# Optimization experiments

Measured on AMD Instinct MI355X. Metric: run time of the kernel, lower is better.

Reference implementation:

```python
import jax, jax.numpy as jnp
import numpy as np

NEG_SLOPE = 0.2
EPS = 1e-16  # PyG softmax denominator epsilon


def add_self_loops(edge_index, num_nodes):
    loop = jnp.arange(num_nodes, dtype=edge_index.dtype)
    src = jnp.concatenate([edge_index[0], loop])
    dst = jnp.concatenate([edge_index[1], loop])
    return src, dst


def gat_conv(x, src, dst, W, att_src, att_dst, bias, num_nodes):
    H, C = att_src.shape
    h = (x @ W).reshape(num_nodes, H, C)            # [N,H,C]
    a_s = jnp.einsum('nhc,hc->nh', h, att_src)      # [N,H]
    a_d = jnp.einsum('nhc,hc->nh', h, att_dst)
    e = jax.nn.leaky_relu(a_s[src] + a_d[dst], NEG_SLOPE)  # [E,H]
    m = jax.ops.segment_max(e, dst, num_segments=num_nodes)
    e = jnp.exp(e - m[dst])
    s = jax.ops.segment_sum(e, dst, num_segments=num_nodes)
    alpha = e / (s[dst] + EPS)                      # [E,H]
    out = jax.ops.segment_sum(h[src] * alpha[:, :, None], dst,
                              num_segments=num_nodes)  # [N,H,C]
    return out.reshape(num_nodes, H * C) + bias


def setup_inputs() -> dict:
    key = jax.random.key(0)
    ks = jax.random.split(key, 10)
    N, E, F, Ch = 50000, 800000, 128, 64
    sc = lambda f: 1.0 / np.sqrt(f)
    return {
        'x': jax.random.normal(ks[0], (N, F), jnp.float32),
        'edge_index': jax.random.randint(ks[1], (2, E), 0, N, jnp.int64),
        'W1': jax.random.normal(ks[2], (F, 4 * Ch), jnp.float32) * sc(F),
        'att_src1': jax.random.normal(ks[3], (4, Ch), jnp.float32) * sc(Ch),
        'att_dst1': jax.random.normal(ks[4], (4, Ch), jnp.float32) * sc(Ch),
        'b1': jnp.zeros((4 * Ch,), jnp.float32),
        'W2': jax.random.normal(ks[5], (4 * Ch, Ch), jnp.float32) * sc(4 * Ch),
        'att_src2': jax.random.normal(ks[6], (1, Ch), jnp.float32) * sc(Ch),
        'att_dst2': jax.random.normal(ks[7], (1, Ch), jnp.float32) * sc(Ch),
        'b2': jnp.zeros((Ch,), jnp.float32),
    }


def reference(x, edge_index, W1, att_src1, att_dst1, b1, W2, att_src2, att_dst2, b2):
    N = x.shape[0]
    src, dst = add_self_loops(edge_index, N)
    # dropout layers are inference no-ops
    h = gat_conv(x, src, dst, W1, att_src1, att_dst1, b1, N)
    h = jax.nn.elu(h)
    out = gat_conv(h, src, dst, W2, att_src2, att_dst2, b2, N)
    return out
```

## Files before the change

### kernel.cpp

```cpp
#include <hip/hip_runtime.h>
#include <hip/hip_bf16.h>
#include <stdint.h>


typedef __attribute__((ext_vector_type(8))) short bf16x8;
typedef __attribute__((ext_vector_type(8))) unsigned short u16x8;
typedef __attribute__((ext_vector_type(4))) float f32x4;

__device__ __forceinline__ float bf2f(__hip_bfloat16 v) { return __bfloat162float(v); }
__device__ __forceinline__ float bfbits2f(unsigned short s) {
  union { uint32_t u; float f; } v; v.u = ((uint32_t)s) << 16; return v.f;
}
__device__ __forceinline__ unsigned short f2bfbits(float f) {
  union { float f; uint32_t u; } v; v.f = f;
  uint32_t u = v.u;
  return (unsigned short)((u + 0x7fffu + ((u >> 16) & 1u)) >> 16);
}

template <bool BF>
__device__ __forceinline__ float loadF(const void* p, size_t i) {
  if (BF) return bf2f(((const __hip_bfloat16*)p)[i]);
  return ((const float*)p)[i];
}
template <bool BF>
__device__ __forceinline__ void storeF(void* p, size_t i, float v) {
  if (BF) ((__hip_bfloat16*)p)[i] = __float2bfloat16(v);
  else    ((float*)p)[i] = v;
}
template <bool I64>
__device__ __forceinline__ int loadI(const void* p, size_t i) {
  if (I64) return (int)((const long long*)p)[i];
  return ((const int*)p)[i];
}
__device__ __forceinline__ float lrelu(float v) { return fmaxf(v, 0.2f * v); }

__global__ void detect_kernel(const uint32_t* __restrict__ xbits,
                              const uint32_t* __restrict__ eibits,
                              int* __restrict__ flags) {
  const int l = threadIdx.x;
  uint32_t u = xbits[l];
  uint32_t e = (u >> 23) & 0xffu;
  bool plausible = (e < 160u && e > 90u) || (u & 0x7fffffffu) == 0u;
  unsigned long long m1 = __ballot(plausible);
  bool z = (eibits[2 * l + 1] == 0u);
  unsigned long long m2 = __ballot(z);
  if (l == 0) {
    flags[0] = (__popcll(m1) < 32) ? 1 : 0;
    flags[1] = (m2 == ~0ULL) ? 1 : 0;
  }
}

__global__ __launch_bounds__(256) void prep_all(
    const void* __restrict__ x, unsigned short* __restrict__ xb, size_t nx,
    const void* __restrict__ W1, unsigned short* __restrict__ w1t, int K1, int N1,
    const void* __restrict__ W2, unsigned short* __restrict__ w2t, int K2, int N2,
    int nb_cast, int nb_t1, const int* __restrict__ flags) {
  const int b = blockIdx.x;
  const bool f = flags[0] != 0;
  if (b < nb_cast) {
    size_t i = ((size_t)b * 256 + threadIdx.x) * 4;
    if (i >= nx) return;
    ushort4 o;
    if (f) {
      o = *(const ushort4*)((const unsigned short*)x + i);
    } else {
      float4 v = *(const float4*)((const float*)x + i);
      o.x = f2bfbits(v.x); o.y = f2bfbits(v.y);
      o.z = f2bfbits(v.z); o.w = f2bfbits(v.w);
    }
    *(ushort4*)(xb + i) = o;
  } else if (b < nb_cast + nb_t1) {
    int idx = (b - nb_cast) * 256 + threadIdx.x;
    if (idx >= K1 * N1) return;
    int k = idx / N1, n = idx - k * N1;
    float v = f ? loadF<true>(W1, idx) : loadF<false>(W1, idx);
    w1t[(size_t)n * K1 + k] = f2bfbits(v);
  } else {
    int idx = (b - nb_cast - nb_t1) * 256 + threadIdx.x;
    if (idx >= K2 * N2) return;
    int k = idx / N2, n = idx - k * N2;
    float v = f ? loadF<true>(W2, idx) : loadF<false>(W2, idx);
    w2t[(size_t)n * K2 + k] = f2bfbits(v);
  }
}

template <int KC, int NT, int HB>
__global__ __launch_bounds__(256, 4) void gemm_mfma_att(
    const unsigned short* __restrict__ A,
    const unsigned short* __restrict__ BT,
    unsigned short* __restrict__ C,
    const void* __restrict__ att_s, const void* __restrict__ att_d,
    float* __restrict__ as_o, float* __restrict__ ad_o,
    float* __restrict__ wself_o,
    int M, int Htot, const int* __restrict__ flags) {
  const int lane = threadIdx.x & 63;
  const int col = lane & 15;
  const int quad = lane >> 4;
  const int m0 = blockIdx.x * 64 + (threadIdx.x >> 6) * 16;
  const int n0 = blockIdx.y * (NT * 16);
  const int NCOL = Htot * 64;

  int gm = m0 + col;
  if (gm > M - 1) gm = M - 1;
  const unsigned short* arow = A + (size_t)gm * KC + quad * 8;
  const unsigned short* bbase = BT + (size_t)(n0 + col) * KC + quad * 8;

  f32x4 acc[NT] = {};
#pragma unroll
  for (int k0 = 0; k0 < KC; k0 += 32) {
    bf16x8 a = *(const bf16x8*)(arow + k0);
#pragma unroll
    for (int s = 0; s < NT; s++) {
      bf16x8 b = *(const bf16x8*)(bbase + (size_t)s * 16 * KC + k0);
      acc[s] = __builtin_amdgcn_mfma_f32_16x16x32_bf16(a, b, acc[s], 0, 0, 0);
    }
  }
#pragma unroll
  for (int s = 0; s < NT; s++)
#pragma unroll
    for (int r = 0; r < 4; r++) {
      int m = m0 + quad * 4 + r;
      if (m < M) C[(size_t)m * NCOL + n0 + s * 16 + col] = f2bfbits(acc[s][r]);
    }
  const int SC = NT / HB;
  const bool f = flags[0] != 0;
#pragma unroll
  for (int h = 0; h < HB; h++) {
    const int gh = blockIdx.y * HB + h;
    float ps[4] = {0.f, 0.f, 0.f, 0.f};
    float pd[4] = {0.f, 0.f, 0.f, 0.f};
#pragma unroll
    for (int j = 0; j < SC; j++) {
      int s = h * SC + j;
      int ci = gh * 64 + j * 16 + col;
      float av = f ? loadF<true>(att_s, ci) : loadF<false>(att_s, ci);
      float dv = f ? loadF<true>(att_d, ci) : loadF<false>(att_d, ci);
#pragma unroll
      for (int r = 0; r < 4; r++) {
        ps[r] += acc[s][r] * av;
        pd[r] += acc[s][r] * dv;
      }
    }
#pragma unroll
    for (int o = 1; o < 16; o <<= 1) {
#pragma unroll
      for (int r = 0; r < 4; r++) {
        ps[r] += __shfl_xor(ps[r], o);
        pd[r] += __shfl_xor(pd[r], o);
      }
    }
    if (col == 0) {
#pragma unroll
      for (int r = 0; r < 4; r++) {
        int m = m0 + quad * 4 + r;
        if (m < M) {
          as_o[m * Htot + gh] = ps[r];
          ad_o[m * Htot + gh] = pd[r];
          wself_o[m * Htot + gh] = __expf(lrelu(ps[r] + pd[r]));
        }
      }
    }
  }
}

__global__ void hist_kernel(const void* __restrict__ ei, int E,
                            int* __restrict__ deg, const int* __restrict__ flags) {
  int e = blockIdx.x * blockDim.x + threadIdx.x;
  if (e >= E) return;
  int d = flags[1] ? loadI<true>(ei, (size_t)E + e) : loadI<false>(ei, (size_t)E + e);
  atomicAdd(&deg[d], 1);
}

__global__ __launch_bounds__(256) void scan_block_sums(const int* __restrict__ deg,
                                                       int* __restrict__ bsum, int n) {
  __shared__ int buf[256];
  const int t = threadIdx.x;
  const int i = blockIdx.x * 256 + t;
  buf[t] = (i < n) ? deg[i] : 0;
  __syncthreads();
  for (int o = 128; o > 0; o >>= 1) {
    if (t < o) buf[t] += buf[t + o];
    __syncthreads();
  }
  if (t == 0) bsum[blockIdx.x] = buf[0];
}

__global__ __launch_bounds__(256) void scan_bsums(int* __restrict__ bsum, int nb) {
  __shared__ int buf[256];
  const int t = threadIdx.x;
  int orig = (t < nb) ? bsum[t] : 0;
  buf[t] = orig;
  __syncthreads();
  for (int o = 1; o < 256; o <<= 1) {
    int v = (t >= o) ? buf[t - o] : 0;
    __syncthreads();
    buf[t] += v;
    __syncthreads();
  }
  if (t < nb) bsum[t] = buf[t] - orig;
}

__global__ __launch_bounds__(256) void scan_finalize(const int* __restrict__ deg,
                                                     const int* __restrict__ bsum,
                                                     int* __restrict__ row_start, int n) {
  __shared__ int buf[256];
  const int t = threadIdx.x;
  const int i = blockIdx.x * 256 + t;
  int v = (i < n) ? deg[i] : 0;
  buf[t] = v;
  __syncthreads();
  for (int o = 1; o < 256; o <<= 1) {
    int x = (t >= o) ? buf[t - o] : 0;
    __syncthreads();
    buf[t] += x;
    __syncthreads();
  }
  if (i < n) row_start[i + 1] = bsum[blockIdx.x] + buf[t];
  if (i == 0) row_start[0] = 0;
}

__global__ void scatter_edges(const void* __restrict__ ei, int E,
                              const int* __restrict__ row_start,
                              int* __restrict__ cursor, int* __restrict__ col_src,
                              int* __restrict__ col_dst,
                              const int* __restrict__ flags) {
  int e = blockIdx.x * blockDim.x + threadIdx.x;
  if (e >= E) return;
  int s, d;
  if (flags[1]) { s = loadI<true>(ei, e);  d = loadI<true>(ei, (size_t)E + e); }
  else          { s = loadI<false>(ei, e); d = loadI<false>(ei, (size_t)E + e); }
  int pos = atomicAdd(&cursor[d], 1);
  int idx = row_start[d] + pos;
  col_src[idx] = s;
  col_dst[idx] = d;
}

__global__ __launch_bounds__(256) void weight4(
    const int* __restrict__ col_src, const int* __restrict__ col_dst,
    const float4* __restrict__ as4, const float4* __restrict__ ad4,
    float4* __restrict__ wbuf, int E) {
  int e = blockIdx.x * 256 + threadIdx.x;
  if (e >= E) return;
  float4 a = as4[col_src[e]];
  float4 b = ad4[col_dst[e]];
  float4 w;
  w.x = __expf(lrelu(a.x + b.x));
  w.y = __expf(lrelu(a.y + b.y));
  w.z = __expf(lrelu(a.z + b.z));
  w.w = __expf(lrelu(a.w + b.w));
  wbuf[e] = w;
}

__global__ __launch_bounds__(256) void weight1(
    const int* __restrict__ col_src, const int* __restrict__ col_dst,
    const float* __restrict__ as_, const float* __restrict__ ad_,
    float* __restrict__ wbuf, int E) {
  int e = blockIdx.x * 256 + threadIdx.x;
  if (e >= E) return;
  wbuf[e] = __expf(lrelu(as_[col_src[e]] + ad_[col_dst[e]]));
}

__global__ __launch_bounds__(256) void aggregate4(
    const unsigned short* __restrict__ h_in,
    const float* __restrict__ wselfA,
    const float* __restrict__ wbuf,
    const int* __restrict__ row_start, const int* __restrict__ col_src,
    const void* __restrict__ bias,
    unsigned short* __restrict__ out,
    int N, const int* __restrict__ flags) {
  const int dst = blockIdx.x * 4 + (threadIdx.x >> 6);
  if (dst >= N) return;
  const int l = threadIdx.x & 63;
  const int j = l & 31;
  const int half = l >> 5;
  const int h = j >> 3;
  const int rs = row_start[dst];
  const int dg = row_start[dst + 1] - rs;
  const float ws = wselfA[dst * 4 + h];

  float a[8];
  {
    u16x8 sv = *(const u16x8*)(h_in + (size_t)dst * 256 + 8 * j);
    const float s = half ? 0.f : ws;
#pragma unroll
    for (int r = 0; r < 8; r++) a[r] = s * bfbits2f(sv[r]);
  }
  float p = 0.f;
#pragma unroll 4
  for (int i = 0; i < dg; i += 2) {
    const int ii = i + half;
    const bool act = ii < dg;
    const int idx = rs + (act ? ii : (dg - 1));
    const int sn = col_src[idx];
    const float w = act ? wbuf[(size_t)idx * 4 + h] : 0.f;
    p += w;
    u16x8 sv = *(const u16x8*)(h_in + (size_t)sn * 256 + 8 * j);
#pragma unroll
    for (int r = 0; r < 8; r++) a[r] += w * bfbits2f(sv[r]);
  }
#pragma unroll
  for (int r = 0; r < 8; r++) a[r] += __shfl_xor(a[r], 32);
  p += __shfl_xor(p, 32);

  if (half == 0) {
    const float inv = 1.0f / (p + ws + 1e-16f);
    const bool f = flags[0] != 0;
    u16x8 ov;
#pragma unroll
    for (int r = 0; r < 8; r++) {
      float b = f ? loadF<true>(bias, 8 * j + r) : loadF<false>(bias, 8 * j + r);
      float o = a[r] * inv + b;
      o = o > 0.f ? o : __expf(o) - 1.f;
      ov[r] = f2bfbits(o);
    }
    *(u16x8*)(out + (size_t)dst * 256 + 8 * j) = ov;
  }
}

__global__ __launch_bounds__(256) void aggregate1(
    const unsigned short* __restrict__ h_in,
    const float* __restrict__ wselfA,
    const float* __restrict__ wbuf,
    const int* __restrict__ row_start, const int* __restrict__ col_src,
    const void* __restrict__ bias,
    void* __restrict__ out, int N, const int* __restrict__ flags) {
  const int dst = blockIdx.x * 4 + (threadIdx.x >> 6);
  if (dst >= N) return;
  const int l = threadIdx.x & 63;
  const int el = l & 7;
  const int slot = l >> 3;
  const int rs = row_start[dst];
  const int dg = row_start[dst + 1] - rs;
  const float ws = wselfA[dst];

  float a[8];
  {
    u16x8 sv = *(const u16x8*)(h_in + (size_t)dst * 64 + 8 * el);
    const float s = (slot == 0) ? ws : 0.f;
#pragma unroll
    for (int r = 0; r < 8; r++) a[r] = s * bfbits2f(sv[r]);
  }
  float p = 0.f;
#pragma unroll 2
  for (int i = slot; i < dg; i += 8) {
    const int sn = col_src[rs + i];
    const float w = wbuf[rs + i];
    p += w;
    u16x8 sv = *(const u16x8*)(h_in + (size_t)sn * 64 + 8 * el);
#pragma unroll
    for (int r = 0; r < 8; r++) a[r] += w * bfbits2f(sv[r]);
  }
#pragma unroll
  for (int o = 8; o < 64; o <<= 1) {
#pragma unroll
    for (int r = 0; r < 8; r++) a[r] += __shfl_xor(a[r], o);
    p += __shfl_xor(p, o);
  }

  if (slot == 0) {
    const float inv = 1.0f / (p + ws + 1e-16f);
    const bool f = flags[0] != 0;
    float o[8];
#pragma unroll
    for (int r = 0; r < 8; r++) {
      float b = f ? loadF<true>(bias, 8 * el + r) : loadF<false>(bias, 8 * el + r);
      o[r] = a[r] * inv + b;
    }
    const size_t ob = (size_t)dst * 64 + 8 * el;
    if (f) {
      u16x8 ov;
#pragma unroll
      for (int r = 0; r < 8; r++) ov[r] = f2bfbits(o[r]);
      *(u16x8*)((unsigned short*)out + ob) = ov;
    } else {
      float4 v0, v1;
      v0.x = o[0]; v0.y = o[1]; v0.z = o[2]; v0.w = o[3];
      v1.x = o[4]; v1.y = o[5]; v1.z = o[6]; v1.w = o[7];
      *(float4*)((float*)out + ob) = v0;
      *(float4*)((float*)out + ob + 4) = v1;
    }
  }
}

extern "C" void kernel_launch(void* const* d_in, const int* in_sizes, int n_in,
                              void* d_out, int out_size, void* d_ws, size_t ws_size,
                              hipStream_t stream) {
  const void* x    = d_in[0];
  const void* ei   = d_in[1];
  const void* W1   = d_in[2];
  const void* as1w = d_in[3];
  const void* ad1w = d_in[4];
  const void* b1   = d_in[5];
  const void* W2   = d_in[6];
  const void* as2w = d_in[7];
  const void* ad2w = d_in[8];
  const void* b2   = d_in[9];

  const int N  = out_size / 64;
  const int F  = in_sizes[0] / N;
  const int E  = in_sizes[1] / 2;
  const int H1 = in_sizes[3] / 64;
  const int D1 = H1 * 64;
  const int D2 = 64;

  size_t off = 0;
  auto alloc = [&](size_t bytes) -> void* {
    void* p = (char*)d_ws + off;
    off += (bytes + 255) & ~(size_t)255;
    return p;
  };
  int* flags = (int*)alloc(2 * sizeof(int));
  __hip_bfloat16* h1 = (__hip_bfloat16*)alloc((size_t)N * D1 * 2);
  __hip_bfloat16* x2 = (__hip_bfloat16*)alloc((size_t)N * D1 * 2);
  __hip_bfloat16* h2 = h1;
  unsigned short* xb  = (unsigned short*)alloc((size_t)N * F * 2);
  unsigned short* w1t = (unsigned short*)alloc((size_t)D1 * F * 2);
  unsigned short* w2t = (unsigned short*)alloc((size_t)D2 * D1 * 2);
  float* as1 = (float*)alloc((size_t)N * H1 * 4);
  float* ad1 = (float*)alloc((size_t)N * H1 * 4);
  float* wself1 = (float*)alloc((size_t)N * H1 * 4);
  float* as2 = (float*)alloc((size_t)N * 4);
  float* ad2 = (float*)alloc((size_t)N * 4);
  float* wself2 = (float*)alloc((size_t)N * 4);
  int* zero_region = (int*)alloc((size_t)2 * N * 4);
  int* deg = zero_region;
  int* cursor = zero_region + N;
  int* row_start = (int*)alloc((size_t)(N + 1) * 4);
  int* col_src = (int*)alloc((size_t)E * 4);
  int* col_dst = (int*)alloc((size_t)E * 4);
  float* wbuf = (float*)alloc((size_t)E * 4 * 4);
  int* bsum = (int*)alloc((size_t)256 * 4);
  (void)ws_size; (void)n_in;

  const int nb = (N + 255) / 256;
  const int eb = (E + 255) / 256;
  const int db = (N + 3) / 4;
  const int gb = (N + 63) / 64;

  detect_kernel<<<1, 64, 0, stream>>>((const uint32_t*)x, (const uint32_t*)ei, flags);
  hipMemsetAsync(zero_region, 0, (size_t)2 * N * 4, stream);
  hist_kernel<<<eb, 256, 0, stream>>>(ei, E, deg, flags);
  scan_block_sums<<<nb, 256, 0, stream>>>(deg, bsum, N);
  scan_bsums<<<1, 256, 0, stream>>>(bsum, nb);
  scan_finalize<<<nb, 256, 0, stream>>>(deg, bsum, row_start, N);
  scatter_edges<<<eb, 256, 0, stream>>>(ei, E, row_start, cursor, col_src, col_dst, flags);

  const size_t nx = (size_t)N * F;
  const int nb_cast = (int)((nx / 4 + 255) / 256);
  const int nb_t1 = (F * D1 + 255) / 256;
  const int nb_t2 = (D1 * D2 + 255) / 256;
  prep_all<<<nb_cast + nb_t1 + nb_t2, 256, 0, stream>>>(
      x, xb, nx, W1, w1t, F, D1, W2, w2t, D1, D2, nb_cast, nb_t1, flags);

  gemm_mfma_att<128, 8, 2><<<dim3(gb, 2), 256, 0, stream>>>(
      xb, w1t, (unsigned short*)h1, as1w, ad1w, as1, ad1, wself1, N, H1, flags);
  weight4<<<eb, 256, 0, stream>>>(col_src, col_dst, (const float4*)as1,
                                  (const float4*)ad1, (float4*)wbuf, E);
  aggregate4<<<db, 256, 0, stream>>>((const unsigned short*)h1, wself1, wbuf,
                                     row_start, col_src, b1,
                                     (unsigned short*)x2, N, flags);

  gemm_mfma_att<256, 4, 1><<<dim3(gb, 1), 256, 0, stream>>>(
      (const unsigned short*)x2, w2t, (unsigned short*)h2, as2w, ad2w,
      as2, ad2, wself2, N, 1, flags);
  weight1<<<eb, 256, 0, stream>>>(col_src, col_dst, as2, ad2, wbuf, E);
  aggregate1<<<db, 256, 0, stream>>>((const unsigned short*)h2, wself2, wbuf,
                                     row_start, col_src, b2, d_out, N, flags);
}
```

Baseline: 349.4 us.

## Slice aggregation across column blocks and store edge weights as per-head planes

Both aggregation kernels become one templated kernel. Each block now handles a 32-column slice of four destination nodes, so layer 1 launches 8x as many blocks and layer 2 launches 2x. Edge weights are written head-major, one plane per head, so each slice reads them contiguously, and each lane now handles four columns with 8 edge slots per wave instead of 2. The goal is more parallelism and smaller per-slice gathers, at the cost of re-reading col_src and the weights once per slice and using narrower 8-byte loads.

```diff
diff --git a/kernel.cpp b/kernel.cpp
--- a/kernel.cpp
+++ b/kernel.cpp
@@ -4,7 +4,6 @@
 
 
 typedef __attribute__((ext_vector_type(8))) short bf16x8;
-typedef __attribute__((ext_vector_type(8))) unsigned short u16x8;
 typedef __attribute__((ext_vector_type(4))) float f32x4;
 
 __device__ __forceinline__ float bf2f(__hip_bfloat16 v) { return __bfloat162float(v); }
@@ -21,11 +20,6 @@
 __device__ __forceinline__ float loadF(const void* p, size_t i) {
   if (BF) return bf2f(((const __hip_bfloat16*)p)[i]);
   return ((const float*)p)[i];
-}
-template <bool BF>
-__device__ __forceinline__ void storeF(void* p, size_t i, float v) {
-  if (BF) ((__hip_bfloat16*)p)[i] = __float2bfloat16(v);
-  else    ((float*)p)[i] = v;
 }
 template <bool I64>
 __device__ __forceinline__ int loadI(const void* p, size_t i) {
@@ -238,17 +232,15 @@
 __global__ __launch_bounds__(256) void weight4(
     const int* __restrict__ col_src, const int* __restrict__ col_dst,
     const float4* __restrict__ as4, const float4* __restrict__ ad4,
-    float4* __restrict__ wbuf, int E) {
+    float* __restrict__ wplanes, int E) {
   int e = blockIdx.x * 256 + threadIdx.x;
   if (e >= E) return;
   float4 a = as4[col_src[e]];
   float4 b = ad4[col_dst[e]];
-  float4 w;
-  w.x = __expf(lrelu(a.x + b.x));
-  w.y = __expf(lrelu(a.y + b.y));
-  w.z = __expf(lrelu(a.z + b.z));
-  w.w = __expf(lrelu(a.w + b.w));
-  wbuf[e] = w;
+  wplanes[e]                 = __expf(lrelu(a.x + b.x));
+  wplanes[(size_t)E + e]     = __expf(lrelu(a.y + b.y));
+  wplanes[(size_t)2 * E + e] = __expf(lrelu(a.z + b.z));
+  wplanes[(size_t)3 * E + e] = __expf(lrelu(a.w + b.w));
 }
 
 __global__ __launch_bounds__(256) void weight1(
@@ -260,124 +252,78 @@
   wbuf[e] = __expf(lrelu(as_[col_src[e]] + ad_[col_dst[e]]));
 }
 
-__global__ __launch_bounds__(256) void aggregate4(
+template <int DCOLS, int NS, bool ELU, bool OUT_DYN>
+__global__ __launch_bounds__(256) void aggregate_sliced(
     const unsigned short* __restrict__ h_in,
     const float* __restrict__ wselfA,
-    const float* __restrict__ wbuf,
+    const float* __restrict__ wplanes,
     const int* __restrict__ row_start, const int* __restrict__ col_src,
     const void* __restrict__ bias,
-    unsigned short* __restrict__ out,
-    int N, const int* __restrict__ flags) {
-  const int dst = blockIdx.x * 4 + (threadIdx.x >> 6);
+    void* __restrict__ out, int N, int E, const int* __restrict__ flags) {
+  constexpr int H = DCOLS / 64;
+  const int slice = blockIdx.x % NS;
+  const int chunk = blockIdx.x / NS;
+  const int dst = chunk * 4 + (threadIdx.x >> 6);
   if (dst >= N) return;
   const int l = threadIdx.x & 63;
-  const int j = l & 31;
-  const int half = l >> 5;
-  const int h = j >> 3;
+  const int slot = l >> 3;
+  const int cl = l & 7;
+  const int h = (slice * 32) >> 6;
+  const int c0 = slice * 32 + cl * 4;
   const int rs = row_start[dst];
   const int dg = row_start[dst + 1] - rs;
-  const float ws = wselfA[dst * 4 + h];
-
-  float a[8];
-  {
-    u16x8 sv = *(const u16x8*)(h_in + (size_t)dst * 256 + 8 * j);
-    const float s = half ? 0.f : ws;
-#pragma unroll
-    for (int r = 0; r < 8; r++) a[r] = s * bfbits2f(sv[r]);
-  }
-  float p = 0.f;
-#pragma unroll 4
-  for (int i = 0; i < dg; i += 2) {
-    const int ii = i + half;
-    const bool act = ii < dg;
-    const int idx = rs + (act ? ii : (dg - 1));
-    const int sn = col_src[idx];
-    const float w = act ? wbuf[(size_t)idx * 4 + h] : 0.f;
-    p += w;
-    u16x8 sv = *(const u16x8*)(h_in + (size_t)sn * 256 + 8 * j);
-#pragma unroll
-    for (int r = 0; r < 8; r++) a[r] += w * bfbits2f(sv[r]);
-  }
-#pragma unroll
-  for (int r = 0; r < 8; r++) a[r] += __shfl_xor(a[r], 32);
-  p += __shfl_xor(p, 32);
-
-  if (half == 0) {
-    const float inv = 1.0f / (p + ws + 1e-16f);
-    const bool f = flags[0] != 0;
-    u16x8 ov;
-#pragma unroll
-    for (int r = 0; r < 8; r++) {
-      float b = f ? loadF<true>(bias, 8 * j + r) : loadF<false>(bias, 8 * j + r);
-      float o = a[r] * inv + b;
-      o = o > 0.f ? o : __expf(o) - 1.f;
-      ov[r] = f2bfbits(o);
-    }
-    *(u16x8*)(out + (size_t)dst * 256 + 8 * j) = ov;
-  }
-}
-
-__global__ __launch_bounds__(256) void aggregate1(
-    const unsigned short* __restrict__ h_in,
-    const float* __restrict__ wselfA,
-    const float* __restrict__ wbuf,
-    const int* __restrict__ row_start, const int* __restrict__ col_src,
-    const void* __restrict__ bias,
-    void* __restrict__ out, int N, const int* __restrict__ flags) {
-  const int dst = blockIdx.x * 4 + (threadIdx.x >> 6);
-  if (dst >= N) return;
-  const int l = threadIdx.x & 63;
-  const int el = l & 7;
-  const int slot = l >> 3;
-  const int rs = row_start[dst];
-  const int dg = row_start[dst + 1] - rs;
-  const float ws = wselfA[dst];
-
-  float a[8];
-  {
-    u16x8 sv = *(const u16x8*)(h_in + (size_t)dst * 64 + 8 * el);
-    const float s = (slot == 0) ? ws : 0.f;
-#pragma unroll
-    for (int r = 0; r < 8; r++) a[r] = s * bfbits2f(sv[r]);
-  }
-  float p = 0.f;
+  const float ws = wselfA[dst * H + h];
+  const float* __restrict__ wp = wplanes + (size_t)h * E;
+
+  float a0 = 0.f, a1 = 0.f, a2 = 0.f, a3 = 0.f, p = 0.f;
+  if (slot == 0) {
+    ushort4 sv = *(const ushort4*)(h_in + (size_t)dst * DCOLS + c0);
+    a0 = ws * bfbits2f(sv.x); a1 = ws * bfbits2f(sv.y);
+    a2 = ws * bfbits2f(sv.z); a3 = ws * bfbits2f(sv.w);
+  }
 #pragma unroll 2
   for (int i = slot; i < dg; i += 8) {
-    const int sn = col_src[rs + i];
-    const float w = wbuf[rs + i];
+    const int idx = rs + i;
+    const int sn = col_src[idx];
+    const float w = wp[idx];
     p += w;
-    u16x8 sv = *(const u16x8*)(h_in + (size_t)sn * 64 + 8 * el);
-#pragma unroll
-    for (int r = 0; r < 8; r++) a[r] += w * bfbits2f(sv[r]);
+    ushort4 sv = *(const ushort4*)(h_in + (size_t)sn * DCOLS + c0);
+    a0 += w * bfbits2f(sv.x); a1 += w * bfbits2f(sv.y);
+    a2 += w * bfbits2f(sv.z); a3 += w * bfbits2f(sv.w);
   }
 #pragma unroll
   for (int o = 8; o < 64; o <<= 1) {
-#pragma unroll
-    for (int r = 0; r < 8; r++) a[r] += __shfl_xor(a[r], o);
-    p += __shfl_xor(p, o);
-  }
-
+    a0 += __shfl_xor(a0, o); a1 += __shfl_xor(a1, o);
+    a2 += __shfl_xor(a2, o); a3 += __shfl_xor(a3, o);
+    p  += __shfl_xor(p, o);
+  }
   if (slot == 0) {
     const float inv = 1.0f / (p + ws + 1e-16f);
     const bool f = flags[0] != 0;
-    float o[8];
-#pragma unroll
-    for (int r = 0; r < 8; r++) {
-      float b = f ? loadF<true>(bias, 8 * el + r) : loadF<false>(bias, 8 * el + r);
-      o[r] = a[r] * inv + b;
-    }
-    const size_t ob = (size_t)dst * 64 + 8 * el;
+    float b0, b1, b2, b3;
     if (f) {
-      u16x8 ov;
-#pragma unroll
-      for (int r = 0; r < 8; r++) ov[r] = f2bfbits(o[r]);
-      *(u16x8*)((unsigned short*)out + ob) = ov;
+      b0 = loadF<true>(bias, c0 + 0); b1 = loadF<true>(bias, c0 + 1);
+      b2 = loadF<true>(bias, c0 + 2); b3 = loadF<true>(bias, c0 + 3);
     } else {
-      float4 v0, v1;
-      v0.x = o[0]; v0.y = o[1]; v0.z = o[2]; v0.w = o[3];
-      v1.x = o[4]; v1.y = o[5]; v1.z = o[6]; v1.w = o[7];
-      *(float4*)((float*)out + ob) = v0;
-      *(float4*)((float*)out + ob + 4) = v1;
+      b0 = loadF<false>(bias, c0 + 0); b1 = loadF<false>(bias, c0 + 1);
+      b2 = loadF<false>(bias, c0 + 2); b3 = loadF<false>(bias, c0 + 3);
+    }
+    float o0 = a0 * inv + b0, o1 = a1 * inv + b1;
+    float o2 = a2 * inv + b2, o3 = a3 * inv + b3;
+    if (ELU) {
+      o0 = o0 > 0.f ? o0 : __expf(o0) - 1.f;
+      o1 = o1 > 0.f ? o1 : __expf(o1) - 1.f;
+      o2 = o2 > 0.f ? o2 : __expf(o2) - 1.f;
+      o3 = o3 > 0.f ? o3 : __expf(o3) - 1.f;
+    }
+    if (OUT_DYN && !f) {
+      float4 v; v.x = o0; v.y = o1; v.z = o2; v.w = o3;
+      *(float4*)((float*)out + (size_t)dst * DCOLS + c0) = v;
+    } else {
+      ushort4 ov;
+      ov.x = f2bfbits(o0); ov.y = f2bfbits(o1);
+      ov.z = f2bfbits(o2); ov.w = f2bfbits(o3);
+      *(ushort4*)((unsigned short*)out + (size_t)dst * DCOLS + c0) = ov;
     }
   }
 }
@@ -455,15 +401,16 @@
   gemm_mfma_att<128, 8, 2><<<dim3(gb, 2), 256, 0, stream>>>(
       xb, w1t, (unsigned short*)h1, as1w, ad1w, as1, ad1, wself1, N, H1, flags);
   weight4<<<eb, 256, 0, stream>>>(col_src, col_dst, (const float4*)as1,
-                                  (const float4*)ad1, (float4*)wbuf, E);
-  aggregate4<<<db, 256, 0, stream>>>((const unsigned short*)h1, wself1, wbuf,
-                                     row_start, col_src, b1,
-                                     (unsigned short*)x2, N, flags);
+                                  (const float4*)ad1, wbuf, E);
+  aggregate_sliced<256, 8, true, false><<<db * 8, 256, 0, stream>>>(
+      (const unsigned short*)h1, wself1, wbuf, row_start, col_src, b1,
+      (void*)x2, N, E, flags);
 
   gemm_mfma_att<256, 4, 1><<<dim3(gb, 1), 256, 0, stream>>>(
       (const unsigned short*)x2, w2t, (unsigned short*)h2, as2w, ad2w,
       as2, ad2, wself2, N, 1, flags);
   weight1<<<eb, 256, 0, stream>>>(col_src, col_dst, as2, ad2, wbuf, E);
-  aggregate1<<<db, 256, 0, stream>>>((const unsigned short*)h2, wself2, wbuf,
-                                     row_start, col_src, b2, d_out, N, flags);
-}
+  aggregate_sliced<64, 2, false, true><<<db * 2, 256, 0, stream>>>(
+      (const unsigned short*)h2, wself2, wbuf, row_start, col_src, b2,
+      d_out, N, E, flags);
+}
```

Result: slower. 456.8 us (+30.7%).
